# Kernel tuning notes

Measured on AMD Instinct MI355X. Metric: run time of the kernel, lower is better.

## Reference

```python
import jax, jax.numpy as jnp
import numpy as np

B, N, D = 8, 2048, 1024
NEG = -1e9


def setup_inputs() -> dict:
    key = jax.random.key(0)
    kx, kl, kq, kk, kv, ko = jax.random.split(key, 6)
    x = jax.random.normal(kx, (B, N, D), dtype=jnp.float32)
    # prefix padding mask: each clip has a random valid length in [N//2, N]
    lengths = jax.random.randint(kl, (B,), N // 2, N + 1)
    mask = jnp.arange(N)[None, :] < lengths[:, None]  # [B, N] bool
    s = 1.0 / np.sqrt(D)
    Wq = jax.random.normal(kq, (D, D), dtype=jnp.float32) * s  # nn.Linear weight [out,in]
    Wk = jax.random.normal(kk, (D, D), dtype=jnp.float32) * s
    Wv = jax.random.normal(kv, (D, D), dtype=jnp.float32) * s
    Wo = jax.random.normal(ko, (D, D), dtype=jnp.float32) * s
    return {"x": x, "mask": mask, "Wq": Wq, "Wk": Wk, "Wv": Wv, "Wo": Wo}


def reference(x, mask, Wq, Wk, Wv, Wo):
    # Linear (no bias): y = x @ W.T
    K = jnp.einsum('bnd,ed->bne', x, Wk)
    Q = jnp.einsum('bnd,ed->bne', x, Wq) * 0.06
    V = jnp.einsum('bnd,ed->bne', x, Wv)
    logits = jnp.einsum('bne,bme->bnm', Q, K)  # [B, N, N]
    # attention_mask = outer product of padding mask (matmul of mask with its transpose)
    attn_mask = mask[:, :, None] & mask[:, None, :]
    logits = jnp.where(attn_mask, logits, NEG)
    att_weights = jax.nn.softmax(logits, axis=-1)
    # dropout (p=0.5) is identity in eval mode
    # y = (V^T @ W)^T  ->  y[b,i,:] = sum_j att[b,j,i] * V[b,j,:]
    y = jnp.einsum('bji,bjd->bid', att_weights, V)
    y = jnp.einsum('bid,ed->bie', y, Wo)
    return (y, att_weights)
```

## Files before the change

kernel.cpp:

```cpp
#include <hip/hip_runtime.h>
#include <math.h>

typedef __attribute__((ext_vector_type(8))) short short8;
typedef __attribute__((ext_vector_type(4))) float f32x4;

namespace {
constexpr int B_ = 8;
constexpr int N_ = 2048;
constexpr int D_ = 1024;
constexpr float NEGV = -1.0e9f;
}

__device__ __forceinline__ unsigned short f2bf(float x) {
    union { float f; unsigned u; } v; v.f = x;
    unsigned u = v.u + 0x7fffu + ((v.u >> 16) & 1u);
    return (unsigned short)(u >> 16);
}

__global__ __launch_bounds__(256)
void k_lengths(const unsigned char* __restrict__ mask, int* __restrict__ L)
{
    const int b = blockIdx.x;
    const int t = threadIdx.x;
    const bool u8 = (mask[1] != 0);
    int cnt = 0;
    if (u8) {
        for (int n = t; n < N_; n += 256)
            cnt += (mask[(size_t)b * N_ + n] != 0) ? 1 : 0;
    } else {
        const int* mi = (const int*)mask;
        for (int n = t; n < N_; n += 256)
            cnt += (mi[(size_t)b * N_ + n] != 0) ? 1 : 0;
    }
    __shared__ int red[256];
    red[t] = cnt;
    __syncthreads();
    for (int s = 128; s > 0; s >>= 1) {
        if (t < s) red[t] += red[t + s];
        __syncthreads();
    }
    if (t == 0) L[b] = red[0];
}

__global__ __launch_bounds__(256)
void convert_bf16(const float* __restrict__ in, unsigned short* __restrict__ out,
                  int n4, float alpha)
{
    const int i = blockIdx.x * 256 + threadIdx.x;
    if (i >= n4) return;
    const float4 v = ((const float4*)in)[i];
    ushort4 o;
    o.x = f2bf(v.x * alpha); o.y = f2bf(v.y * alpha);
    o.z = f2bf(v.z * alpha); o.w = f2bf(v.w * alpha);
    ((ushort4*)out)[i] = o;
}

template <int OUT_MODE>
__global__ __launch_bounds__(512, 2)
void gemm_nt_256(const unsigned short* __restrict__ A, int lda, long strideA,
                 const unsigned short* __restrict__ Bm, int ldb, long strideB,
                 void* __restrict__ Cout, int ldc, long strideC,
                 int K, const int* __restrict__ Lp)
{
    __shared__ __attribute__((aligned(16))) short As[4][8192];
    __shared__ __attribute__((aligned(16))) short Bs[4][8192];

    const int tid  = threadIdx.x;
    const int lane = tid & 63;
    const int wave = tid >> 6;
    const int wr   = wave >> 2;
    const int wc   = wave & 3;

    const unsigned gx   = gridDim.x;
    const unsigned gxy  = gx * gridDim.y;
    const unsigned total = gxy * gridDim.z;
    const unsigned orig = blockIdx.x + gx * blockIdx.y + gxy * blockIdx.z;
    unsigned wg = orig;
    if ((total & 7u) == 0u)
        wg = (orig & 7u) * (total >> 3) + (orig >> 3);
    const unsigned bz  = wg / gxy;
    const unsigned rem = wg - bz * gxy;
    const unsigned byy = rem / gx;
    const unsigned bxx = rem - byy * gx;

    const int b  = (int)bz;
    const int m0 = (int)byy * 256;
    const int n0 = (int)bxx * 256;

    int Lb = 0;
    if (OUT_MODE == 2) {
        Lb = Lp[b];
        if (m0 >= Lb) return;
        if (n0 >= Lb) {
            float* C = (float*)Cout + (long)b * strideC;
            const float4 nv = make_float4(NEGV, NEGV, NEGV, NEGV);
            const int rl = tid >> 6;
            const int c4 = (tid & 63) * 4;
#pragma unroll
            for (int l = 0; l < 32; ++l)
                *(float4*)(C + (long)(m0 + l * 8 + rl) * ldc + n0 + c4) = nv;
            return;
        }
    }

    const unsigned short* Ab = A  + (long)b * strideA;
    const unsigned short* Bb = Bm + (long)b * strideB;

    const int srow = tid >> 2;
    const int sseg = ((tid & 3) ^ ((tid >> 3) & 3)) * 8;
    const unsigned short* gA = Ab + (long)(m0 + srow) * lda + sseg;
    const unsigned short* gB = Bb + (long)(n0 + srow) * ldb + sseg;
    const int ldst = (tid & ~63) * 8;

    const int q  = lane >> 4, r = lane & 15;
    const int arb = (wr * 128 + r) * 32;
    const int brb = (wc * 64 + r) * 32;
    const int pk  = (q ^ ((r >> 1) & 3)) * 8;

    const int NT = K >> 5;

    short8 aH[4];
    short8 bQ[4];
    f32x4  acc[8][4] = {};

#define STAGE_A(dd, kt) do {                                                   \
    __builtin_amdgcn_global_load_lds(                                          \
        (const __attribute__((address_space(1))) void*)(gA + (long)(kt)*32),   \
        (__attribute__((address_space(3))) void*)(&As[dd][ldst]), 16, 0, 0);   \
    __builtin_amdgcn_global_load_lds(                                          \
        (const __attribute__((address_space(1))) void*)(gA + (long)128*lda + (long)(kt)*32), \
        (__attribute__((address_space(3))) void*)(&As[dd][4096 + ldst]), 16, 0, 0);          \
} while (0)

#define STAGE_B(dd, kt) do {                                                   \
    __builtin_amdgcn_global_load_lds(                                          \
        (const __attribute__((address_space(1))) void*)(gB + (long)(kt)*32),   \
        (__attribute__((address_space(3))) void*)(&Bs[dd][ldst]), 16, 0, 0);   \
    __builtin_amdgcn_global_load_lds(                                          \
        (const __attribute__((address_space(1))) void*)(gB + (long)128*ldb + (long)(kt)*32), \
        (__attribute__((address_space(3))) void*)(&Bs[dd][4096 + ldst]), 16, 0, 0);          \
} while (0)

#define RD_A_H(dd, mh) do {                                                    \
    _Pragma("unroll") for (int mr_ = 0; mr_ < 4; ++mr_)                        \
        aH[mr_] = *(const short8*)&As[dd][arb + ((mh)*4 + mr_) * 512 + pk];    \
} while (0)

#define RD_B_ALL(dd) do {                                                      \
    _Pragma("unroll") for (int nr_ = 0; nr_ < 4; ++nr_)                        \
        bQ[nr_] = *(const short8*)&Bs[dd][brb + nr_ * 512 + pk];               \
} while (0)

#define BARX __builtin_amdgcn_s_barrier()
#define WAIT_LGKM0 do { asm volatile("s_waitcnt lgkmcnt(0)" ::: "memory"); \
                        __builtin_amdgcn_sched_barrier(0); } while (0)
#define WAIT_VM0   do { asm volatile("s_waitcnt vmcnt(0)"   ::: "memory"); \
                        __builtin_amdgcn_sched_barrier(0); } while (0)
#define WAIT_VM4   do { asm volatile("s_waitcnt vmcnt(4)"   ::: "memory"); \
                        __builtin_amdgcn_sched_barrier(0); } while (0)
#define WAIT_VM8   do { asm volatile("s_waitcnt vmcnt(8)"   ::: "memory"); \
                        __builtin_amdgcn_sched_barrier(0); } while (0)

#define MFMA_H(mh) do {                                                        \
    __builtin_amdgcn_s_setprio(1);                                             \
    _Pragma("unroll") for (int mr_ = 0; mr_ < 4; ++mr_)                        \
    _Pragma("unroll") for (int nr_ = 0; nr_ < 4; ++nr_)                        \
        acc[(mh)*4 + mr_][nr_] = __builtin_amdgcn_mfma_f32_16x16x32_bf16(      \
            aH[mr_], bQ[nr_], acc[(mh)*4 + mr_][nr_], 0, 0, 0);                \
    __builtin_amdgcn_s_setprio(0);                                             \
} while (0)

    STAGE_B(0, 0); STAGE_A(0, 0);
    STAGE_B(1, 1); STAGE_A(1, 1);
    STAGE_B(2, 2); STAGE_A(2, 2);
    WAIT_VM8; BARX;

    for (int kt = 0; kt < NT; ++kt) {
        const int d  = kt & 3;
        const int dn = (kt + 3) & 3;
        RD_A_H(d, 0); RD_B_ALL(d);
        if (kt + 3 < NT) STAGE_B(dn, kt + 3);
        BARX; WAIT_LGKM0; MFMA_H(0); BARX;
        RD_A_H(d, 1);
        if (kt + 3 < NT) { STAGE_A(dn, kt + 3); WAIT_VM8; }
        else if (kt + 2 < NT) { WAIT_VM4; }
        else { WAIT_VM0; }
        BARX; WAIT_LGKM0; MFMA_H(1); BARX;
    }

#undef STAGE_A
#undef STAGE_B
#undef RD_A_H
#undef RD_B_ALL
#undef BARX
#undef WAIT_LGKM0
#undef WAIT_VM0
#undef WAIT_VM4
#undef WAIT_VM8
#undef MFMA_H

    const int rbase = m0 + wr * 128;
    const int cbase = n0 + wc * 64;
    if (OUT_MODE == 1) {
        unsigned short* C = (unsigned short*)Cout + (long)b * strideC;
#pragma unroll
        for (int mt = 0; mt < 8; ++mt)
#pragma unroll
            for (int nt = 0; nt < 4; ++nt)
#pragma unroll
                for (int rr = 0; rr < 4; ++rr) {
                    const int grow = rbase + mt * 16 + q * 4 + rr;
                    const int gcol = cbase + nt * 16 + r;
                    C[(long)grow * ldc + gcol] = f2bf(acc[mt][nt][rr]);
                }
    } else if (OUT_MODE == 0) {
        float* C = (float*)Cout + (long)b * strideC;
#pragma unroll
        for (int mt = 0; mt < 8; ++mt)
#pragma unroll
            for (int nt = 0; nt < 4; ++nt)
#pragma unroll
                for (int rr = 0; rr < 4; ++rr) {
                    const int grow = rbase + mt * 16 + q * 4 + rr;
                    const int gcol = cbase + nt * 16 + r;
                    C[(long)grow * ldc + gcol] = acc[mt][nt][rr];
                }
    } else {
        float* C = (float*)Cout + (long)b * strideC;
#pragma unroll
        for (int mt = 0; mt < 8; ++mt)
#pragma unroll
            for (int nt = 0; nt < 4; ++nt)
#pragma unroll
                for (int rr = 0; rr < 4; ++rr) {
                    const int grow = rbase + mt * 16 + q * 4 + rr;
                    const int gcol = cbase + nt * 16 + r;
                    const float val = (grow < Lb && gcol < Lb) ? acc[mt][nt][rr] : NEGV;
                    C[(long)grow * ldc + gcol] = val;
                }
    }
}

__global__ __launch_bounds__(256)
void softmax_rows(float* __restrict__ Att, const int* __restrict__ Lp)
{
    const size_t row = blockIdx.x;
    const int i = (int)(row & (N_ - 1));
    const int b = (int)(row >> 11);
    float* p = Att + row * (size_t)N_;
    const int t = threadIdx.x;

    if (i >= Lp[b]) {
        const float c = 1.0f / 2048.0f;
        const float4 cv = make_float4(c, c, c, c);
        *(float4*)(p + t * 4)        = cv;
        *(float4*)(p + 1024 + t * 4) = cv;
        return;
    }

    float4 v0 = *(float4*)(p + t * 4);
    float4 v1 = *(float4*)(p + 1024 + t * 4);

    float mx = fmaxf(fmaxf(fmaxf(v0.x, v0.y), fmaxf(v0.z, v0.w)),
                     fmaxf(fmaxf(v1.x, v1.y), fmaxf(v1.z, v1.w)));
#pragma unroll
    for (int o = 32; o > 0; o >>= 1) mx = fmaxf(mx, __shfl_xor(mx, o, 64));

    __shared__ float red[8];
    const int wv = t >> 6;
    if ((t & 63) == 0) red[wv] = mx;
    __syncthreads();
    mx = fmaxf(fmaxf(red[0], red[1]), fmaxf(red[2], red[3]));

    float e[8];
    e[0] = expf(v0.x - mx); e[1] = expf(v0.y - mx);
    e[2] = expf(v0.z - mx); e[3] = expf(v0.w - mx);
    e[4] = expf(v1.x - mx); e[5] = expf(v1.y - mx);
    e[6] = expf(v1.z - mx); e[7] = expf(v1.w - mx);
    float s = ((e[0] + e[1]) + (e[2] + e[3])) + ((e[4] + e[5]) + (e[6] + e[7]));
#pragma unroll
    for (int o = 32; o > 0; o >>= 1) s += __shfl_xor(s, o, 64);
    if ((t & 63) == 0) red[4 + wv] = s;
    __syncthreads();
    const float inv = 1.0f / (red[4] + red[5] + red[6] + red[7]);

    *(float4*)(p + t * 4)        = make_float4(e[0] * inv, e[1] * inv, e[2] * inv, e[3] * inv);
    *(float4*)(p + 1024 + t * 4) = make_float4(e[4] * inv, e[5] * inv, e[6] * inv, e[7] * inv);
}

__global__ __launch_bounds__(256)
void transpose_att_bf16(const float* __restrict__ att, unsigned short* __restrict__ attT)
{
    __shared__ float tile[64][65];
    const int b  = blockIdx.z;
    const int j0 = blockIdx.y * 64;
    const int i0 = blockIdx.x * 64;
    const float* src = att + (long)b * N_ * N_;
    unsigned short* dst = attT + (long)b * N_ * N_;
    const int t = threadIdx.x;
#pragma unroll
    for (int l = 0; l < 4; ++l) {
        const int idx = t + l * 256;
        const int jj = idx >> 4;
        const int i4 = (idx & 15) * 4;
        const float4 v = *(const float4*)(src + (long)(j0 + jj) * N_ + i0 + i4);
        tile[i4 + 0][jj] = v.x;
        tile[i4 + 1][jj] = v.y;
        tile[i4 + 2][jj] = v.z;
        tile[i4 + 3][jj] = v.w;
    }
    __syncthreads();
#pragma unroll
    for (int l = 0; l < 4; ++l) {
        const int idx = t + l * 256;
        const int ii = idx >> 4;
        const int j4 = (idx & 15) * 4;
        ushort4 o;
        o.x = f2bf(tile[ii][j4 + 0]);
        o.y = f2bf(tile[ii][j4 + 1]);
        o.z = f2bf(tile[ii][j4 + 2]);
        o.w = f2bf(tile[ii][j4 + 3]);
        *(ushort4*)(dst + (long)(i0 + ii) * N_ + j0 + j4) = o;
    }
}

__global__ __launch_bounds__(256)
void transpose_v_bf16(const unsigned short* __restrict__ qkv, unsigned short* __restrict__ vt)
{
    __shared__ unsigned short tile[64][68];
    const int j0 = blockIdx.x * 64;
    const int d0 = blockIdx.y * 64;
    const int t = threadIdx.x;
#pragma unroll
    for (int l = 0; l < 4; ++l) {
        const int idx = t + l * 256;
        const int jj = idx >> 4;
        const int d4 = (idx & 15) * 4;
        const ushort4 v = *(const ushort4*)(qkv + (long)(j0 + jj) * 3072 + 2048 + d0 + d4);
        tile[d4 + 0][jj] = v.x;
        tile[d4 + 1][jj] = v.y;
        tile[d4 + 2][jj] = v.z;
        tile[d4 + 3][jj] = v.w;
    }
    __syncthreads();
#pragma unroll
    for (int l = 0; l < 4; ++l) {
        const int idx = t + l * 256;
        const int dd = idx >> 4;
        const int j4 = (idx & 15) * 4;
        ushort4 o;
        o.x = tile[dd][j4 + 0];
        o.y = tile[dd][j4 + 1];
        o.z = tile[dd][j4 + 2];
        o.w = tile[dd][j4 + 3];
        *(ushort4*)(vt + (long)(d0 + dd) * 16384 + j0 + j4) = o;
    }
}

extern "C" void kernel_launch(void* const* d_in, const int* in_sizes, int n_in,
                              void* d_out, int out_size, void* d_ws, size_t ws_size,
                              hipStream_t stream)
{
    const float* x  = (const float*)d_in[0];
    const unsigned char* mask = (const unsigned char*)d_in[1];
    const float* Wq = (const float*)d_in[2];
    const float* Wk = (const float*)d_in[3];
    const float* Wv = (const float*)d_in[4];
    const float* Wo = (const float*)d_in[5];

    float* y   = (float*)d_out;
    float* att = (float*)d_out + (size_t)B_ * N_ * D_;

    char* ws = (char*)d_ws;
    int* L = (int*)ws;
    unsigned short* Wqkvb = (unsigned short*)(ws + 256);
    unsigned short* Wob   = Wqkvb + 3145728;
    unsigned short* xb    = Wob + 1048576;
    unsigned short* QKVb  = xb + 16777216;
    unsigned short* VT    = QKVb + 50331648;
    unsigned short* attT  = QKVb;
    unsigned short* ctx   = xb;

    const dim3 blk(256);
    const dim3 blk512(512);
    const long NN = (long)N_ * N_;
    const long ND = (long)N_ * D_;
    const long NQ = (long)N_ * 3072;

    k_lengths<<<dim3(B_), blk, 0, stream>>>(mask, L);

    convert_bf16<<<dim3(16384), blk, 0, stream>>>(x,  xb,  4194304, 1.0f);
    convert_bf16<<<dim3(1024),  blk, 0, stream>>>(Wq, Wqkvb,           262144, 0.06f);
    convert_bf16<<<dim3(1024),  blk, 0, stream>>>(Wk, Wqkvb + 1048576, 262144, 1.0f);
    convert_bf16<<<dim3(1024),  blk, 0, stream>>>(Wv, Wqkvb + 2097152, 262144, 1.0f);
    convert_bf16<<<dim3(1024),  blk, 0, stream>>>(Wo, Wob,             262144, 1.0f);

    gemm_nt_256<1><<<dim3(12, 64, 1), blk512, 0, stream>>>(
        xb, D_, 0, Wqkvb, D_, 0, QKVb, 3072, 0, D_, nullptr);

    transpose_v_bf16<<<dim3(256, 16), blk, 0, stream>>>(QKVb, VT);

    gemm_nt_256<2><<<dim3(8, 8, B_), blk512, 0, stream>>>(
        QKVb, 3072, NQ, QKVb + 1024, 3072, NQ, att, N_, NN, D_, L);

    softmax_rows<<<dim3(B_ * N_), blk, 0, stream>>>(att, L);

    transpose_att_bf16<<<dim3(32, 32, B_), blk, 0, stream>>>(att, attT);

    gemm_nt_256<1><<<dim3(4, 8, B_), blk512, 0, stream>>>(
        attT, N_, NN, VT, B_ * N_, N_, ctx, D_, ND, N_, nullptr);

    gemm_nt_256<0><<<dim3(4, 64, 1), blk512, 0, stream>>>(
        ctx, D_, 0, Wob, D_, 0, y, D_, 0, D_, nullptr);
}
```

Measured before the change: 619.4 us.

## Merge half-step GEMM main loop into one k-step with fewer barriers

Restructures the bf16 MFMA GEMM main loop so each k-tile issues both A and B prefetches up front, waits once, and then reads all eight A fragments and four B fragments from LDS. It then runs all 32 MFMAs in one block. This cuts the barriers per k-iteration from four to two and removes the split of A reads into halves, aiming to reduce synchronization stalls. The cost is higher register pressure from holding eight A fragments, and less interleaving of LDS reads with MFMA work, which may expose LDS latency.

```diff
diff --git a/kernel.cpp b/kernel.cpp
--- a/kernel.cpp
+++ b/kernel.cpp
@@ -119,7 +119,7 @@
 
     const int NT = K >> 5;
 
-    short8 aH[4];
+    short8 aQ[8];
     short8 bQ[4];
     f32x4  acc[8][4] = {};
 
@@ -139,16 +139,6 @@
     __builtin_amdgcn_global_load_lds(                                          \
         (const __attribute__((address_space(1))) void*)(gB + (long)128*ldb + (long)(kt)*32), \
         (__attribute__((address_space(3))) void*)(&Bs[dd][4096 + ldst]), 16, 0, 0);          \
-} while (0)
-
-#define RD_A_H(dd, mh) do {                                                    \
-    _Pragma("unroll") for (int mr_ = 0; mr_ < 4; ++mr_)                        \
-        aH[mr_] = *(const short8*)&As[dd][arb + ((mh)*4 + mr_) * 512 + pk];    \
-} while (0)
-
-#define RD_B_ALL(dd) do {                                                      \
-    _Pragma("unroll") for (int nr_ = 0; nr_ < 4; ++nr_)                        \
-        bQ[nr_] = *(const short8*)&Bs[dd][brb + nr_ * 512 + pk];               \
 } while (0)
 
 #define BARX __builtin_amdgcn_s_barrier()
@@ -161,43 +151,53 @@
 #define WAIT_VM8   do { asm volatile("s_waitcnt vmcnt(8)"   ::: "memory"); \
                         __builtin_amdgcn_sched_barrier(0); } while (0)
 
-#define MFMA_H(mh) do {                                                        \
-    __builtin_amdgcn_s_setprio(1);                                             \
-    _Pragma("unroll") for (int mr_ = 0; mr_ < 4; ++mr_)                        \
-    _Pragma("unroll") for (int nr_ = 0; nr_ < 4; ++nr_)                        \
-        acc[(mh)*4 + mr_][nr_] = __builtin_amdgcn_mfma_f32_16x16x32_bf16(      \
-            aH[mr_], bQ[nr_], acc[(mh)*4 + mr_][nr_], 0, 0, 0);                \
-    __builtin_amdgcn_s_setprio(0);                                             \
-} while (0)
-
     STAGE_B(0, 0); STAGE_A(0, 0);
     STAGE_B(1, 1); STAGE_A(1, 1);
     STAGE_B(2, 2); STAGE_A(2, 2);
-    WAIT_VM8; BARX;
+    WAIT_VM8;
 
     for (int kt = 0; kt < NT; ++kt) {
         const int d  = kt & 3;
         const int dn = (kt + 3) & 3;
-        RD_A_H(d, 0); RD_B_ALL(d);
-        if (kt + 3 < NT) STAGE_B(dn, kt + 3);
-        BARX; WAIT_LGKM0; MFMA_H(0); BARX;
-        RD_A_H(d, 1);
-        if (kt + 3 < NT) { STAGE_A(dn, kt + 3); WAIT_VM8; }
-        else if (kt + 2 < NT) { WAIT_VM4; }
-        else { WAIT_VM0; }
-        BARX; WAIT_LGKM0; MFMA_H(1); BARX;
+
+        if (kt + 3 < NT) {
+            STAGE_B(dn, kt + 3);
+            STAGE_A(dn, kt + 3);
+            WAIT_VM8;
+        } else if (kt + 3 == NT) {
+            WAIT_VM4;
+        } else {
+            WAIT_VM0;
+        }
+        BARX;
+
+#pragma unroll
+        for (int nr = 0; nr < 4; ++nr)
+            bQ[nr] = *(const short8*)&Bs[d][brb + nr * 512 + pk];
+#pragma unroll
+        for (int mr = 0; mr < 8; ++mr)
+            aQ[mr] = *(const short8*)&As[d][arb + mr * 512 + pk];
+
+        __builtin_amdgcn_s_setprio(1);
+#pragma unroll
+        for (int mr = 0; mr < 8; ++mr)
+#pragma unroll
+            for (int nr = 0; nr < 4; ++nr)
+                acc[mr][nr] = __builtin_amdgcn_mfma_f32_16x16x32_bf16(
+                    aQ[mr], bQ[nr], acc[mr][nr], 0, 0, 0);
+        __builtin_amdgcn_s_setprio(0);
+
+        WAIT_LGKM0;
+        BARX;
     }
 
 #undef STAGE_A
 #undef STAGE_B
-#undef RD_A_H
-#undef RD_B_ALL
 #undef BARX
 #undef WAIT_LGKM0
 #undef WAIT_VM0
 #undef WAIT_VM4
 #undef WAIT_VM8
-#undef MFMA_H
 
     const int rbase = m0 + wr * 128;
     const int cbase = n0 + wc * 64;
```

Measured after the change: 680.1 us. 1.1x slower.
